# Performance work log

Measured on AMD Instinct MI355X. Metric: run time of the kernel, lower is better.

## Reference

```python
import jax, jax.numpy as jnp
import numpy as np

N_NODES = 100000


def gcn_conv(x, edge_index, W, b):
    # PyG GCNConv: add self-loops, symmetric normalization D^-1/2 (A+I) D^-1/2, then linear.
    n = x.shape[0]
    loop = jnp.arange(n, dtype=edge_index.dtype)
    src = jnp.concatenate([edge_index[0], loop])
    dst = jnp.concatenate([edge_index[1], loop])
    deg = jax.ops.segment_sum(jnp.ones_like(dst, dtype=x.dtype), dst, num_segments=n)
    dinv = jnp.where(deg > 0, jax.lax.rsqrt(deg), 0.0)
    norm = dinv[src] * dinv[dst]                      # [E+N]
    h = x @ W                                          # [N, out]
    msg = h[src] * norm[:, None]                       # gather + scale
    out = jax.ops.segment_sum(msg, dst, num_segments=n)  # scatter-add
    return out + b


def forward_one(x, edge_index, W1, b1, W2, b2, fc_w, fc_b):
    x = jax.nn.relu(gcn_conv(x, edge_index, W1, b1))
    x = jax.nn.relu(gcn_conv(x, edge_index, W2, b2))
    x = jnp.mean(x, axis=0)                            # [hidden]
    return x @ fc_w.T + fc_b


def setup_inputs() -> dict:
    key = jax.random.key(0)
    ks = jax.random.split(key, 10)
    d_in, d_h = 64, 64
    E = 1600000
    s = 1.0 / np.sqrt(d_in)
    return {
        "x1": jax.random.normal(ks[0], (N_NODES, d_in), jnp.float32),
        "x2": jax.random.normal(ks[1], (N_NODES, d_in), jnp.float32),
        "edge_index1": jax.random.randint(ks[2], (2, E), 0, N_NODES, jnp.int32),
        "edge_index2": jax.random.randint(ks[3], (2, E), 0, N_NODES, jnp.int32),
        "W1": jax.random.normal(ks[4], (d_in, d_h), jnp.float32) * s,
        "b1": jnp.zeros((d_h,), jnp.float32),
        "W2": jax.random.normal(ks[5], (d_h, d_h), jnp.float32) * s,
        "b2": jnp.zeros((d_h,), jnp.float32),
        "fc_w": jax.random.normal(ks[6], (d_h, d_h), jnp.float32) * s,
        "fc_b": jnp.zeros((d_h,), jnp.float32),
    }


def reference(x1, x2, edge_index1, edge_index2, W1, b1, W2, b2, fc_w, fc_b):
    out1 = forward_one(x1, edge_index1, W1, b1, W2, b2, fc_w, fc_b)
    out2 = forward_one(x2, edge_index2, W1, b1, W2, b2, fc_w, fc_b)
    return (out1, out2)
```

## Files before the change

kernel.cpp:

```cpp
#include <hip/hip_runtime.h>


#define TPB    256
#define CHUNK  128
#define SHIFT  7
#define KMAX   1024
#define CAP    2560
#define EPB    8192
#define CPAD   16

typedef __attribute__((ext_vector_type(8))) short short8;
typedef __attribute__((ext_vector_type(4))) float f32x4;
typedef __attribute__((ext_vector_type(2))) float float2v;

struct Ctx {
    const float* X; const int* esrc; const int* edst;
    unsigned int* temp; unsigned short* Ab; unsigned char* Hs;
    unsigned int* csr; int* row_ptr; int* degA; float* dinv; int* cursorG;
    float* P; float* P2; float* outp;
};

__device__ __forceinline__ unsigned short f2bf(float x) {
    union { float f; unsigned int i; } c; c.f = x;
    unsigned int r = c.i + 0x7FFFu + ((c.i >> 16) & 1u);
    return (unsigned short)(r >> 16);
}
__device__ __forceinline__ unsigned char f2fp8(float x) {
    int p = __builtin_amdgcn_cvt_pk_fp8_f32(x, x, 0, false);
    return (unsigned char)(p & 0xFF);
}
__device__ __forceinline__ float2v up8lo(unsigned int w) {
    return __builtin_amdgcn_cvt_pk_f32_fp8(w, false);
}
__device__ __forceinline__ float2v up8hi(unsigned int w) {
    return __builtin_amdgcn_cvt_pk_f32_fp8(w, true);
}

__global__ void k_prepW2(const float* __restrict__ W1, const float* __restrict__ W2,
                         unsigned short* __restrict__ Wt1, unsigned short* __restrict__ Wt2) {
    const float* W = blockIdx.x ? W2 : W1;
    unsigned short* Wt = blockIdx.x ? Wt2 : Wt1;
    for (int i = threadIdx.x; i < 64 * 64; i += 256) {
        int n = i >> 6, k = i & 63;
        Wt[i] = f2bf(W[k * 64 + n]);
    }
}

__global__ void k_zeroCur(Ctx c0, Ctx c1, int nb0, int K, int N) {
    int b = blockIdx.x; Ctx c = c0;
    if (b >= nb0) { c = c1; b -= nb0; }
    int i = b * blockDim.x + threadIdx.x;
    if (i < K) c.cursorG[i * CPAD] = 0;
    if (b == 0 && threadIdx.x < 64) c.Hs[(size_t)N * 64 + threadIdx.x] = 0;
}

__global__ __launch_bounds__(1024) void k_binA(Ctx c0, Ctx c1, int nb0, int E, int K) {
    __shared__ int cnt[KMAX];
    __shared__ int ofs[KMAX];
    __shared__ int segBase[KMAX];
    __shared__ unsigned int sorted[EPB];
    __shared__ unsigned short bkt[EPB];
    int b = blockIdx.x; Ctx c = c0;
    if (b >= nb0) { c = c1; b -= nb0; }
    int tid = threadIdx.x;
    cnt[tid] = 0;
    __syncthreads();
    int base = b * EPB;
    int tot = E - base; if (tot > EPB) tot = EPB;
#pragma unroll
    for (int k = 0; k < EPB / 1024; ++k) {
        int e = base + k * 1024 + tid;
        if (e < E) atomicAdd(&cnt[c.edst[e] >> SHIFT], 1);
    }
    __syncthreads();
    int v = cnt[tid];
    segBase[tid] = v;
    __syncthreads();
#pragma unroll
    for (int off = 1; off < 1024; off <<= 1) {
        int t = (tid >= off) ? segBase[tid - off] : 0;
        __syncthreads();
        segBase[tid] += t;
        __syncthreads();
    }
    ofs[tid] = segBase[tid] - v;
    __syncthreads();
    if (tid < K) {
        segBase[tid] = v ? atomicAdd(&c.cursorG[tid * CPAD], v) : 0;
    } else {
        segBase[tid] = 0;
    }
    cnt[tid] = 0;
    __syncthreads();
#pragma unroll
    for (int k = 0; k < EPB / 1024; ++k) {
        int e = base + k * 1024 + tid;
        if (e < E) {
            int d = c.edst[e];
            int bk = d >> SHIFT;
            int r = atomicAdd(&cnt[bk], 1);
            int p = ofs[bk] + r;
            sorted[p] = ((unsigned int)(d & (CHUNK - 1)) << 17) | (unsigned int)c.esrc[e];
            bkt[p] = (unsigned short)bk;
        }
    }
    __syncthreads();
    for (int p = tid; p < tot; p += 1024) {
        unsigned int vv = sorted[p];
        int bk = bkt[p];
        int pos = segBase[bk] + (p - ofs[bk]);
        if (pos < CAP) c.temp[(size_t)bk * CAP + pos] = vv;
    }
}

__global__ __launch_bounds__(256) void k_csrb(Ctx c0, Ctx c1, int nb0, int N) {
    __shared__ int deg[CHUNK];
    __shared__ int lofs[CHUNK];
    __shared__ int cur[CHUNK];
    int b = blockIdx.x; Ctx c = c0;
    if (b >= nb0) { c = c1; b -= nb0; }
    int tid = threadIdx.x;
    if (tid < CHUNK) deg[tid] = 0;
    __syncthreads();
    int cnt = c.cursorG[b * CPAD]; if (cnt > CAP) cnt = CAP;
    const size_t tb = (size_t)b * CAP;
    for (int i = tid; i < cnt; i += 256) atomicAdd(&deg[c.temp[tb + i] >> 17], 1);
    __syncthreads();
    if (tid < CHUNK) lofs[tid] = deg[tid];
    __syncthreads();
#pragma unroll
    for (int off = 1; off < CHUNK; off <<= 1) {
        int t = (tid < CHUNK && tid >= off) ? lofs[tid - off] : 0;
        __syncthreads();
        if (tid < CHUNK) lofs[tid] += t;
        __syncthreads();
    }
    int base = b * CAP;
    if (tid < CHUNK) {
        int excl = lofs[tid] - deg[tid];
        lofs[tid] = excl;
        cur[tid] = 0;
        int node = b * CHUNK + tid;
        if (node < N) {
            c.row_ptr[node] = base + excl;
            c.degA[node] = deg[tid];
            c.dinv[node] = rsqrtf((float)deg[tid] + 1.0f);
        }
    }
    __syncthreads();
    for (int i = tid; i < cnt; i += 256) {
        unsigned int p = c.temp[tb + i];
        int dl = p >> 17;
        int rank = atomicAdd(&cur[dl], 1);
        c.csr[base + lofs[dl] + rank] = (p & 0x1FFFFu) << 6;
    }
}

__device__ __forceinline__ void mfma_tail(short8 a0, short8 a1,
                                          const unsigned short* __restrict__ Wt,
                                          unsigned char* __restrict__ Hs,
                                          int row0, int r, int q, int N) {
    short8 bfrag[4][2];
#pragma unroll
    for (int ct = 0; ct < 4; ++ct)
#pragma unroll
        for (int kb = 0; kb < 2; ++kb)
            bfrag[ct][kb] = *(const short8*)(Wt + (ct * 16 + r) * 64 + q * 8 + 32 * kb);
    f32x4 acc[4];
#pragma unroll
    for (int ct = 0; ct < 4; ++ct) {
        acc[ct] = (f32x4){0.0f, 0.0f, 0.0f, 0.0f};
        acc[ct] = __builtin_amdgcn_mfma_f32_16x16x32_bf16(a0, bfrag[ct][0], acc[ct], 0, 0, 0);
        acc[ct] = __builtin_amdgcn_mfma_f32_16x16x32_bf16(a1, bfrag[ct][1], acc[ct], 0, 0, 0);
    }
#pragma unroll
    for (int reg = 0; reg < 4; ++reg) {
        int row = row0 + q * 4 + reg;
        if (row < N) {
            size_t base = (size_t)row * 64 + r;
#pragma unroll
            for (int ct = 0; ct < 4; ++ct)
                Hs[base + ct * 16] = f2fp8(acc[ct][reg]);
        }
    }
}

__global__ __launch_bounds__(256) void k_gemm1(Ctx c0, Ctx c1, int nb0,
                                               const unsigned short* __restrict__ Wt,
                                               int nTiles, int N) {
    int b = blockIdx.x; Ctx c = c0;
    if (b >= nb0) { c = c1; b -= nb0; }
    int wave = threadIdx.x >> 6, lane = threadIdx.x & 63;
    int tile = b * 4 + wave;
    if (tile >= nTiles) return;
    int r = lane & 15, q = lane >> 4;
    int row0 = tile * 16;
    int row = row0 + r;
    int rr = row < N ? row : N - 1;
    float d = c.dinv[rr];
    const float* xrow = c.X + (size_t)rr * 64 + q * 8;
    short8 a0, a1;
#pragma unroll
    for (int j = 0; j < 8; ++j) a0[j] = (short)f2bf(xrow[j] * d);
#pragma unroll
    for (int j = 0; j < 8; ++j) a1[j] = (short)f2bf(xrow[32 + j] * d);
    mfma_tail(a0, a1, Wt, c.Hs, row0, r, q, N);
}

__global__ __launch_bounds__(256) void k_gemm2(Ctx c0, Ctx c1, int nb0,
                                               const unsigned short* __restrict__ Wt,
                                               int nTiles, int N) {
    int b = blockIdx.x; Ctx c = c0;
    if (b >= nb0) { c = c1; b -= nb0; }
    int wave = threadIdx.x >> 6, lane = threadIdx.x & 63;
    int tile = b * 4 + wave;
    if (tile >= nTiles) return;
    int r = lane & 15, q = lane >> 4;
    int row0 = tile * 16;
    const unsigned short* xrow = c.Ab + (size_t)(row0 + r) * 64 + q * 8;
    short8 a0 = *(const short8*)(xrow);
    short8 a1 = *(const short8*)(xrow + 32);
    mfma_tail(a0, a1, Wt, c.Hs, row0, r, q, N);
}

__device__ __forceinline__ void agg_map(int bi, int nb0, int swz,
                                        const Ctx& c0, const Ctx& c1,
                                        Ctx& c, int& b) {
    if (swz) {
        int graph = (bi >> 2) & 1;
        b = ((bi >> 3) << 2) | (bi & 3);
        c = graph ? c1 : c0;
    } else {
        b = bi; c = c0;
        if (b >= nb0) { c = c1; b -= nb0; }
    }
}

__device__ __forceinline__ void agg_node2(const unsigned char* __restrict__ Hs,
                                          const unsigned int* __restrict__ csr,
                                          int beg, int deg, int maxd, int lane,
                                          unsigned int sent, float2v* acc) {
    int hbase = lane & 32;
    int hl = lane & 31;
    int g = (lane >> 4) & 1;
    unsigned int s4 = (unsigned int)((lane & 15) * 4);
    for (int base = 0; base < maxd; base += 32) {
        unsigned int idx = (base + hl < deg) ? csr[beg + base + hl] : sent;
        int mW = maxd - base; if (mW > 32) mW = 32;
        for (int t = 0; t < mW; t += 16) {
            unsigned int h[8];
#pragma unroll
            for (int u = 0; u < 8; ++u) {
                int slot = t + 2 * u + g;
                unsigned int su = (unsigned int)__shfl((int)idx, hbase + slot, 64);
                h[u] = *(const unsigned int*)(Hs + (su | s4));
            }
#pragma unroll
            for (int u = 0; u < 8; ++u) {
                acc[0] += up8lo(h[u]); acc[1] += up8hi(h[u]);
            }
        }
    }
#pragma unroll
    for (int k = 0; k < 2; ++k) {
        float2v o;
        o.x = __shfl_xor(acc[k].x, 16, 64); o.y = __shfl_xor(acc[k].y, 16, 64);
        acc[k] += o;
    }
}

__global__ __launch_bounds__(256) void k_agg1(Ctx c0, Ctx c1, int nb0, int swz,
                                              const float* __restrict__ bias, int n) {
    Ctx c; int b;
    agg_map(blockIdx.x, nb0, swz, c0, c1, c, b);
    int wave = threadIdx.x >> 6, lane = threadIdx.x & 63;
    int h = lane >> 5;
    int node = b * 8 + wave * 2 + h;
    int nd = node < n ? node : 0;
    int beg = c.row_ptr[nd];
    int deg = (node < n) ? c.degA[nd] : 0;
    int od = __shfl_xor(deg, 32, 64);
    int maxd = deg > od ? deg : od;
    float2v acc[2] = {{0.f, 0.f}, {0.f, 0.f}};
    agg_node2(c.Hs, c.csr, beg, deg, maxd, lane, (unsigned int)n << 6, acc);
    if (((lane >> 4) & 1) == 0 && node < n) {
        int s = lane & 15;
        unsigned int hv = *(const unsigned int*)(c.Hs + (size_t)node * 64 + s * 4);
        float2v h0 = up8lo(hv), h1 = up8hi(hv);
        float4 bb = *(const float4*)(bias + s * 4);
        float d = c.dinv[node];
        float v0 = fmaxf(bb.x + d * (acc[0].x + h0.x), 0.0f) * d;
        float v1 = fmaxf(bb.y + d * (acc[0].y + h0.y), 0.0f) * d;
        float v2 = fmaxf(bb.z + d * (acc[1].x + h1.x), 0.0f) * d;
        float v3 = fmaxf(bb.w + d * (acc[1].y + h1.y), 0.0f) * d;
        ushort4 o;
        o.x = f2bf(v0); o.y = f2bf(v1); o.z = f2bf(v2); o.w = f2bf(v3);
        *(ushort4*)(c.Ab + (size_t)node * 64 + s * 4) = o;
    }
}

__global__ __launch_bounds__(256) void k_agg2(Ctx c0, Ctx c1, int nb0, int swz,
                                              const float* __restrict__ bias, int n) {
    __shared__ float red[8 * 64];
    Ctx c; int b;
    agg_map(blockIdx.x, nb0, swz, c0, c1, c, b);
    int wave = threadIdx.x >> 6, lane = threadIdx.x & 63;
    int h = lane >> 5;
    int node = b * 8 + wave * 2 + h;
    int nd = node < n ? node : 0;
    int beg = c.row_ptr[nd];
    int deg = (node < n) ? c.degA[nd] : 0;
    int od = __shfl_xor(deg, 32, 64);
    int maxd = deg > od ? deg : od;
    float2v acc[2] = {{0.f, 0.f}, {0.f, 0.f}};
    agg_node2(c.Hs, c.csr, beg, deg, maxd, lane, (unsigned int)n << 6, acc);
    if (((lane >> 4) & 1) == 0) {
        int s = lane & 15;
        float4 v = {0.f, 0.f, 0.f, 0.f};
        if (node < n) {
            unsigned int hv = *(const unsigned int*)(c.Hs + (size_t)node * 64 + s * 4);
            float2v h0 = up8lo(hv), h1 = up8hi(hv);
            float4 bb = *(const float4*)(bias + s * 4);
            float d = c.dinv[node];
            v.x = fmaxf(bb.x + d * (acc[0].x + h0.x), 0.0f);
            v.y = fmaxf(bb.y + d * (acc[0].y + h0.y), 0.0f);
            v.z = fmaxf(bb.z + d * (acc[1].x + h1.x), 0.0f);
            v.w = fmaxf(bb.w + d * (acc[1].y + h1.y), 0.0f);
        }
        *(float4*)(&red[(wave * 2 + h) * 64 + s * 4]) = v;
    }
    __syncthreads();
    if (threadIdx.x < 64) {
        float acc8 = 0.0f;
#pragma unroll
        for (int r = 0; r < 8; ++r) acc8 += red[r * 64 + threadIdx.x];
        c.P[(size_t)b * 64 + threadIdx.x] = acc8;
    }
}

__global__ void k_colsum(Ctx c0, Ctx c1, int nb0, int rows) {
    int b = blockIdx.x; Ctx c = c0;
    if (b >= nb0) { c = c1; b -= nb0; }
    int f = threadIdx.x;
    float acc = 0.0f;
    for (int r = b; r < rows; r += nb0) acc += c.P[(size_t)r * 64 + f];
    c.P2[b * 64 + f] = acc;
}

__global__ void k_fc(Ctx c0, Ctx c1, const float* __restrict__ fcw,
                     const float* __restrict__ fcb, int n) {
    Ctx c = blockIdx.x ? c1 : c0;
    __shared__ float S[64];
    int j = threadIdx.x;
    float s = 0.0f;
    for (int r = 0; r < 256; ++r) s += c.P2[r * 64 + j];
    S[j] = s;
    __syncthreads();
    float inv = 1.0f / (float)n;
    float acc = fcb[j];
#pragma unroll
    for (int k = 0; k < 64; ++k) acc += (S[k] * inv) * fcw[j * 64 + k];
    c.outp[j] = acc;
}

extern "C" void kernel_launch(void* const* d_in, const int* in_sizes, int n_in,
                              void* d_out, int out_size, void* d_ws, size_t ws_size,
                              hipStream_t stream) {
    const float* x[2]  = {(const float*)d_in[0], (const float*)d_in[1]};
    const int*   ei[2] = {(const int*)d_in[2], (const int*)d_in[3]};
    const float* W1  = (const float*)d_in[4];
    const float* b1  = (const float*)d_in[5];
    const float* W2  = (const float*)d_in[6];
    const float* b2  = (const float*)d_in[7];
    const float* fcw = (const float*)d_in[8];
    const float* fcb = (const float*)d_in[9];
    float* out = (float*)d_out;

    const int N  = in_sizes[0] / 64;
    const int E  = in_sizes[2] / 2;
    const int NF = N * 64;
    const int K  = (N + CHUNK - 1) / CHUNK;
    const int gGm = (N + 7) / 8;
    const int nTiles = (N + 15) / 16;
    const int gMf = (nTiles + 3) / 4;
    const int gBin = (E + EPB - 1) / EPB;
    const int gK  = (K + TPB - 1) / TPB;

    auto al = [](size_t x) { return (x + 127) & ~(size_t)127; };
    size_t tempB = (size_t)K * CAP * 4;
    size_t abB   = ((size_t)NF + 64) * 2;
    size_t szRegion = al(tempB > abB ? tempB : abB);
    size_t szHs  = al((size_t)NF + 64);
    size_t szCsr = al((size_t)K * CAP * 4);
    size_t szRp  = al((size_t)N * 4);
    size_t szDeg = al((size_t)N * 4);
    size_t szDi  = al((size_t)N * 4);
    size_t szCu  = al((size_t)K * CPAD * 4);
    size_t szP   = al((size_t)gGm * 64 * 4);
    size_t szP2  = al((size_t)256 * 64 * 4);
    size_t setB  = szRegion + szHs + szCsr + szRp + szDeg + szDi + szCu + szP + szP2;
    size_t wtB   = 2 * al(64 * 64 * 2);
    bool batched = ws_size >= wtB + 2 * setB;

    char* base = (char*)d_ws;
    unsigned short* Wt1 = (unsigned short*)base;
    unsigned short* Wt2 = (unsigned short*)(base + al(64 * 64 * 2));

    auto mkctx = [&](int g, char* p) {
        Ctx c;
        c.X = x[g]; c.esrc = ei[g]; c.edst = ei[g] + E;
        c.temp = (unsigned int*)p; c.Ab = (unsigned short*)p; p += szRegion;
        c.Hs = (unsigned char*)p; p += szHs;
        c.csr = (unsigned int*)p; p += szCsr;
        c.row_ptr = (int*)p; p += szRp;
        c.degA = (int*)p; p += szDeg;
        c.dinv = (float*)p; p += szDi;
        c.cursorG = (int*)p; p += szCu;
        c.P = (float*)p; p += szP;
        c.P2 = (float*)p;
        c.outp = out + g * 64;
        return c;
    };
    char* set0 = base + wtB;
    Ctx c0 = mkctx(0, set0);
    Ctx c1 = mkctx(1, batched ? set0 + setB : set0);

    k_prepW2<<<2, 256, 0, stream>>>(W1, W2, Wt1, Wt2);

    auto pipe = [&](Ctx A, Ctx B, int mult) {
        int swz = (mult == 2 && (gGm & 3) == 0) ? 1 : 0;
        k_zeroCur<<<mult * gK, TPB, 0, stream>>>(A, B, gK, K, N);
        k_binA<<<mult * gBin, 1024, 0, stream>>>(A, B, gBin, E, K);
        k_csrb<<<mult * K, 256, 0, stream>>>(A, B, K, N);
        k_gemm1<<<mult * gMf, 256, 0, stream>>>(A, B, gMf, Wt1, nTiles, N);
        k_agg1<<<mult * gGm, 256, 0, stream>>>(A, B, gGm, swz, b1, N);
        k_gemm2<<<mult * gMf, 256, 0, stream>>>(A, B, gMf, Wt2, nTiles, N);
        k_agg2<<<mult * gGm, 256, 0, stream>>>(A, B, gGm, swz, b2, N);
        k_colsum<<<mult * 256, 64, 0, stream>>>(A, B, 256, gGm);
        k_fc<<<mult, 64, 0, stream>>>(A, B, fcw, fcb, N);
    };

    if (batched) {
        pipe(c0, c1, 2);
    } else {
        pipe(c0, c0, 1);
        pipe(c1, c1, 1);
    }
}
```

Baseline: 318.1 us.

## Fuse second-layer GEMM into first aggregation kernel, emit fp8 H2 directly

The first aggregation kernel now stages its 8 bf16 output rows per block in shared memory and multiplies them by W2 with MFMA, writing the fp8 second-layer features straight into a new Hs2 buffer. This removes the separate gemm2 launch and the bf16 intermediate round trip through global memory. The aggregation inner loop is also restructured to issue up to 16 gathers per 32-edge window in one unrolled block instead of two 8-gather chunks. In exchange each block pads a 16-row MFMA with only 8 valid rows, wasting half the matrix work, and adds a block-wide barrier plus byte-granular scattered stores to Hs2.

```diff
diff --git a/kernel.cpp b/kernel.cpp
--- a/kernel.cpp
+++ b/kernel.cpp
@@ -15,7 +15,7 @@
 
 struct Ctx {
     const float* X; const int* esrc; const int* edst;
-    unsigned int* temp; unsigned short* Ab; unsigned char* Hs;
+    unsigned int* temp; unsigned char* Hs2; unsigned char* Hs;
     unsigned int* csr; int* row_ptr; int* degA; float* dinv; int* cursorG;
     float* P; float* P2; float* outp;
 };
@@ -207,22 +207,6 @@
     mfma_tail(a0, a1, Wt, c.Hs, row0, r, q, N);
 }
 
-__global__ __launch_bounds__(256) void k_gemm2(Ctx c0, Ctx c1, int nb0,
-                                               const unsigned short* __restrict__ Wt,
-                                               int nTiles, int N) {
-    int b = blockIdx.x; Ctx c = c0;
-    if (b >= nb0) { c = c1; b -= nb0; }
-    int wave = threadIdx.x >> 6, lane = threadIdx.x & 63;
-    int tile = b * 4 + wave;
-    if (tile >= nTiles) return;
-    int r = lane & 15, q = lane >> 4;
-    int row0 = tile * 16;
-    const unsigned short* xrow = c.Ab + (size_t)(row0 + r) * 64 + q * 8;
-    short8 a0 = *(const short8*)(xrow);
-    short8 a1 = *(const short8*)(xrow + 32);
-    mfma_tail(a0, a1, Wt, c.Hs, row0, r, q, N);
-}
-
 __device__ __forceinline__ void agg_map(int bi, int nb0, int swz,
                                         const Ctx& c0, const Ctx& c1,
                                         Ctx& c, int& b) {
@@ -247,18 +231,17 @@
     for (int base = 0; base < maxd; base += 32) {
         unsigned int idx = (base + hl < deg) ? csr[beg + base + hl] : sent;
         int mW = maxd - base; if (mW > 32) mW = 32;
-        for (int t = 0; t < mW; t += 16) {
-            unsigned int h[8];
-#pragma unroll
-            for (int u = 0; u < 8; ++u) {
-                int slot = t + 2 * u + g;
-                unsigned int su = (unsigned int)__shfl((int)idx, hbase + slot, 64);
-                h[u] = *(const unsigned int*)(Hs + (su | s4));
-            }
-#pragma unroll
-            for (int u = 0; u < 8; ++u) {
-                acc[0] += up8lo(h[u]); acc[1] += up8hi(h[u]);
-            }
+        unsigned int h[16];
+#pragma unroll
+        for (int u = 0; u < 16; ++u) {
+            if (2 * u >= mW) break;
+            unsigned int su = (unsigned int)__shfl((int)idx, hbase + 2 * u + g, 64);
+            h[u] = *(const unsigned int*)(Hs + (su | s4));
+        }
+#pragma unroll
+        for (int u = 0; u < 16; ++u) {
+            if (2 * u >= mW) break;
+            acc[0] += up8lo(h[u]); acc[1] += up8hi(h[u]);
         }
     }
 #pragma unroll
@@ -270,7 +253,10 @@
 }
 
 __global__ __launch_bounds__(256) void k_agg1(Ctx c0, Ctx c1, int nb0, int swz,
-                                              const float* __restrict__ bias, int n) {
+                                              const float* __restrict__ bias,
+                                              const unsigned short* __restrict__ Wt2,
+                                              int n) {
+    __shared__ unsigned short As[8][64];
     Ctx c; int b;
     agg_map(blockIdx.x, nb0, swz, c0, c1, c, b);
     int wave = threadIdx.x >> 6, lane = threadIdx.x & 63;
@@ -281,21 +267,45 @@
     int deg = (node < n) ? c.degA[nd] : 0;
     int od = __shfl_xor(deg, 32, 64);
     int maxd = deg > od ? deg : od;
+    if (b == 0 && threadIdx.x < 64) c.Hs2[(size_t)n * 64 + threadIdx.x] = 0;
     float2v acc[2] = {{0.f, 0.f}, {0.f, 0.f}};
     agg_node2(c.Hs, c.csr, beg, deg, maxd, lane, (unsigned int)n << 6, acc);
-    if (((lane >> 4) & 1) == 0 && node < n) {
+    if (((lane >> 4) & 1) == 0) {
         int s = lane & 15;
-        unsigned int hv = *(const unsigned int*)(c.Hs + (size_t)node * 64 + s * 4);
-        float2v h0 = up8lo(hv), h1 = up8hi(hv);
-        float4 bb = *(const float4*)(bias + s * 4);
-        float d = c.dinv[node];
-        float v0 = fmaxf(bb.x + d * (acc[0].x + h0.x), 0.0f) * d;
-        float v1 = fmaxf(bb.y + d * (acc[0].y + h0.y), 0.0f) * d;
-        float v2 = fmaxf(bb.z + d * (acc[1].x + h1.x), 0.0f) * d;
-        float v3 = fmaxf(bb.w + d * (acc[1].y + h1.y), 0.0f) * d;
-        ushort4 o;
-        o.x = f2bf(v0); o.y = f2bf(v1); o.z = f2bf(v2); o.w = f2bf(v3);
-        *(ushort4*)(c.Ab + (size_t)node * 64 + s * 4) = o;
+        ushort4 o = {0, 0, 0, 0};
+        if (node < n) {
+            unsigned int hv = *(const unsigned int*)(c.Hs + (size_t)node * 64 + s * 4);
+            float2v h0 = up8lo(hv), h1 = up8hi(hv);
+            float4 bb = *(const float4*)(bias + s * 4);
+            float d = c.dinv[node];
+            o.x = f2bf(fmaxf(bb.x + d * (acc[0].x + h0.x), 0.0f) * d);
+            o.y = f2bf(fmaxf(bb.y + d * (acc[0].y + h0.y), 0.0f) * d);
+            o.z = f2bf(fmaxf(bb.z + d * (acc[1].x + h1.x), 0.0f) * d);
+            o.w = f2bf(fmaxf(bb.w + d * (acc[1].y + h1.y), 0.0f) * d);
+        }
+        *(ushort4*)(&As[wave * 2 + h][s * 4]) = o;
+    }
+    __syncthreads();
+    {
+        int r = lane & 15, q = lane >> 4;
+        short8 a0 = {}, a1 = {};
+        if (r < 8) {
+            a0 = *(const short8*)(&As[r][q * 8]);
+            a1 = *(const short8*)(&As[r][q * 8 + 32]);
+        }
+        const unsigned short* wp = Wt2 + (wave * 16 + r) * 64 + q * 8;
+        short8 b0 = *(const short8*)(wp);
+        short8 b1 = *(const short8*)(wp + 32);
+        f32x4 acc2 = {0.0f, 0.0f, 0.0f, 0.0f};
+        acc2 = __builtin_amdgcn_mfma_f32_16x16x32_bf16(a0, b0, acc2, 0, 0, 0);
+        acc2 = __builtin_amdgcn_mfma_f32_16x16x32_bf16(a1, b1, acc2, 0, 0, 0);
+#pragma unroll
+        for (int reg = 0; reg < 4; ++reg) {
+            int l = q * 4 + reg;
+            int row = b * 8 + l;
+            if (l < 8 && row < n)
+                c.Hs2[(size_t)row * 64 + wave * 16 + r] = f2fp8(acc2[reg]);
+        }
     }
 }
 
@@ -313,12 +323,12 @@
     int od = __shfl_xor(deg, 32, 64);
     int maxd = deg > od ? deg : od;
     float2v acc[2] = {{0.f, 0.f}, {0.f, 0.f}};
-    agg_node2(c.Hs, c.csr, beg, deg, maxd, lane, (unsigned int)n << 6, acc);
+    agg_node2(c.Hs2, c.csr, beg, deg, maxd, lane, (unsigned int)n << 6, acc);
     if (((lane >> 4) & 1) == 0) {
         int s = lane & 15;
         float4 v = {0.f, 0.f, 0.f, 0.f};
         if (node < n) {
-            unsigned int hv = *(const unsigned int*)(c.Hs + (size_t)node * 64 + s * 4);
+            unsigned int hv = *(const unsigned int*)(c.Hs2 + (size_t)node * 64 + s * 4);
             float2v h0 = up8lo(hv), h1 = up8hi(hv);
             float4 bb = *(const float4*)(bias + s * 4);
             float d = c.dinv[node];
@@ -388,8 +398,8 @@
 
     auto al = [](size_t x) { return (x + 127) & ~(size_t)127; };
     size_t tempB = (size_t)K * CAP * 4;
-    size_t abB   = ((size_t)NF + 64) * 2;
-    size_t szRegion = al(tempB > abB ? tempB : abB);
+    size_t hs2B  = (size_t)NF + 64;
+    size_t szRegion = al(tempB > hs2B ? tempB : hs2B);
     size_t szHs  = al((size_t)NF + 64);
     size_t szCsr = al((size_t)K * CAP * 4);
     size_t szRp  = al((size_t)N * 4);
@@ -409,7 +419,7 @@
     auto mkctx = [&](int g, char* p) {
         Ctx c;
         c.X = x[g]; c.esrc = ei[g]; c.edst = ei[g] + E;
-        c.temp = (unsigned int*)p; c.Ab = (unsigned short*)p; p += szRegion;
+        c.temp = (unsigned int*)p; c.Hs2 = (unsigned char*)p; p += szRegion;
         c.Hs = (unsigned char*)p; p += szHs;
         c.csr = (unsigned int*)p; p += szCsr;
         c.row_ptr = (int*)p; p += szRp;
@@ -433,8 +443,7 @@
         k_binA<<<mult * gBin, 1024, 0, stream>>>(A, B, gBin, E, K);
         k_csrb<<<mult * K, 256, 0, stream>>>(A, B, K, N);
         k_gemm1<<<mult * gMf, 256, 0, stream>>>(A, B, gMf, Wt1, nTiles, N);
-        k_agg1<<<mult * gGm, 256, 0, stream>>>(A, B, gGm, swz, b1, N);
-        k_gemm2<<<mult * gMf, 256, 0, stream>>>(A, B, gMf, Wt2, nTiles, N);
+        k_agg1<<<mult * gGm, 256, 0, stream>>>(A, B, gGm, swz, b1, Wt2, N);
         k_agg2<<<mult * gGm, 256, 0, stream>>>(A, B, gGm, swz, b2, N);
         k_colsum<<<mult * 256, 64, 0, stream>>>(A, B, 256, gGm);
         k_fc<<<mult, 64, 0, stream>>>(A, B, fcw, fcb, N);
```

New measurement: 310.5 us. 2.4% less time.
